# Performance work log

Hardware: AMD Instinct MI355X
Metric: run time of the kernel (lower is better)

The kernel has to match this reference:

```python
import jax, jax.numpy as jnp
import numpy as np

KH, KW = 5, 5  # filter_size


def setup_inputs() -> dict:
    key = jax.random.key(0)
    k1, k2 = jax.random.split(key)
    n, c, t, h, w = 1, 3, 25, 128, 128
    filter_prod = KH * KW  # 25
    up_sq = 16
    x = jax.random.normal(k1, (n, c, t, h, w), dtype=jnp.float32)
    filters = jax.random.uniform(k2, (n, filter_prod, up_sq, t, h, w), dtype=jnp.float32)
    return {"x": x, "filters": filters}


def reference(x, filters):
    # x: (n, 3, t, h, w); filters: (n, kh*kw, up_sq, t, h, w)
    n, c, t, h, w = x.shape
    up_sq = filters.shape[2]
    ph, pw = KH // 2, KW // 2
    # The torch module's 25 one-hot grouped conv2d calls are exactly im2col:
    # patch k = a*KW + b is x shifted by (a-ph, b-pw) with zero padding.
    xp = jnp.pad(x, ((0, 0), (0, 0), (0, 0), (ph, ph), (pw, pw)))
    patches = jnp.stack(
        [xp[:, :, :, a:a + h, b:b + w] for a in range(KH) for b in range(KW)],
        axis=-1,
    )  # (n, 3, t, h, w, kh*kw)
    out = jnp.einsum('ncthwk,nkuthw->ncuthw', patches, filters)
    # (n, 3, up_sq, t, h, w) -> (n, 3*up_sq, t, h, w)
    return out.reshape(n, c * up_sq, t, h, w)
```

## Files before the change

kernel.cpp:

```cpp
#include <hip/hip_runtime.h>


#define T_ 25
#define H_ 128
#define W_ 128
#define C_ 3
#define U_ 16
#define KH_ 5
#define KW_ 5
#define HW_ (H_ * W_)
#define THW_ (T_ * HW_)

#define BLOCK_PIX 256
#define LROWS 6
#define LCOLS 132

__global__ __launch_bounds__(256) void duf_kernel(
    const float* __restrict__ x,
    const float* __restrict__ filt,
    float* __restrict__ out)
{
    __shared__ __align__(16) float xs[C_ * LROWS * LCOLS];

    const int tid = threadIdx.x;
    const int P0  = blockIdx.x * BLOCK_PIX;
    const int t   = P0 / HW_;
    const int h0  = (P0 - t * HW_) / W_;

    const float* xt = x + (size_t)t * HW_;
    for (int idx = tid; idx < C_ * LROWS * LCOLS; idx += 256) {
        const int c   = idx / (LROWS * LCOLS);
        const int rem = idx - c * (LROWS * LCOLS);
        const int r   = rem / LCOLS;
        const int col = rem - r * LCOLS;
        const int gh  = h0 - 2 + r;
        const int gw  = col - 2;
        float v = 0.f;
        if ((unsigned)gh < (unsigned)H_ && (unsigned)gw < (unsigned)W_)
            v = xt[(size_t)c * THW_ + gh * W_ + gw];
        xs[idx] = v;
    }
    __syncthreads();

    const int lane = tid & 63;
    const int uq   = tid >> 6;
    const int p0   = P0 + lane * 4;
    const int lrow = lane >> 5;
    const int w0   = (lane & 31) * 4;

    float4 acc[C_][4];
#pragma unroll
    for (int c = 0; c < C_; ++c)
#pragma unroll
        for (int u = 0; u < 4; ++u)
            acc[c][u] = make_float4(0.f, 0.f, 0.f, 0.f);

    const float* fb = filt + (size_t)(uq * 4) * THW_ + p0;

#pragma unroll 1
    for (int a = 0; a < KH_; ++a) {
        float xr[C_][8];
#pragma unroll
        for (int c = 0; c < C_; ++c) {
            const float4* s =
                (const float4*)&xs[(c * LROWS + lrow + a) * LCOLS + w0];
            const float4 lo = s[0];
            const float4 hi = s[1];
            xr[c][0] = lo.x; xr[c][1] = lo.y; xr[c][2] = lo.z; xr[c][3] = lo.w;
            xr[c][4] = hi.x; xr[c][5] = hi.y; xr[c][6] = hi.z; xr[c][7] = hi.w;
        }
        const float* fa = fb + (size_t)a * (KW_ * U_) * THW_;
#pragma unroll
        for (int b = 0; b < KW_; ++b) {
#pragma unroll
            for (int u = 0; u < 4; ++u) {
                const float4 f =
                    *(const float4*)(fa + (size_t)(b * U_ + u) * THW_);
#pragma unroll
                for (int c = 0; c < C_; ++c) {
                    acc[c][u].x += xr[c][b + 0] * f.x;
                    acc[c][u].y += xr[c][b + 1] * f.y;
                    acc[c][u].z += xr[c][b + 2] * f.z;
                    acc[c][u].w += xr[c][b + 3] * f.w;
                }
            }
        }
    }

#pragma unroll
    for (int c = 0; c < C_; ++c)
#pragma unroll
        for (int u = 0; u < 4; ++u)
            *(float4*)(out + (size_t)(c * U_ + uq * 4 + u) * THW_ + p0) =
                acc[c][u];
}

extern "C" void kernel_launch(void* const* d_in, const int* in_sizes, int n_in,
                              void* d_out, int out_size, void* d_ws, size_t ws_size,
                              hipStream_t stream) {
    const float* x = (const float*)d_in[0];
    const float* filt = (const float*)d_in[1];
    float* out = (float*)d_out;
    dim3 grid(THW_ / BLOCK_PIX);
    dim3 block(256);
    duf_kernel<<<grid, block, 0, stream>>>(x, filt, out);
}
```

Before: 854.4 us.

## Tile 16-row spans per block with one upsample per wave and nontemporal loads

Each block now covers a 16-row span of one frame for a group of four upsample channels, and each wave handles a single upsample channel over eight pixel sub-tiles. Before, each block covered 256 pixels and each wave handled four channels. The x halo in shared memory is reused across more pixels, and the grid shrinks to 800 blocks. Filter loads and output stores now use nontemporal builtins so the large streaming traffic bypasses cache retention. The risks are fewer blocks for the GPU's many CUs, more redundant x halo loads (four channel-group blocks reload the same span), and more registers per thread.

```diff
diff --git a/kernel.cpp b/kernel.cpp
--- a/kernel.cpp
+++ b/kernel.cpp
@@ -1,5 +1,7 @@
 #include <hip/hip_runtime.h>
 
+
+typedef float f4 __attribute__((ext_vector_type(4)));
 
 #define T_ 25
 #define H_ 128
@@ -11,9 +13,11 @@
 #define HW_ (H_ * W_)
 #define THW_ (T_ * HW_)
 
-#define BLOCK_PIX 256
-#define LROWS 6
-#define LCOLS 132
+#define SPAN_ROWS 16
+#define SPAN_PX (SPAN_ROWS * W_)
+#define NSPAN (H_ / SPAN_ROWS)
+#define LROWS (SPAN_ROWS + KH_ - 1)
+#define LCOLS (W_ + 4)
 
 __global__ __launch_bounds__(256) void duf_kernel(
     const float* __restrict__ x,
@@ -22,10 +26,12 @@
 {
     __shared__ __align__(16) float xs[C_ * LROWS * LCOLS];
 
+    const int bid = blockIdx.x;
+    const int ug  = bid & 3;
+    const int sp  = (bid >> 2) & (NSPAN - 1);
+    const int t   = bid >> 5;
+
     const int tid = threadIdx.x;
-    const int P0  = blockIdx.x * BLOCK_PIX;
-    const int t   = P0 / HW_;
-    const int h0  = (P0 - t * HW_) / W_;
 
     const float* xt = x + (size_t)t * HW_;
     for (int idx = tid; idx < C_ * LROWS * LCOLS; idx += 256) {
@@ -33,7 +39,7 @@
         const int rem = idx - c * (LROWS * LCOLS);
         const int r   = rem / LCOLS;
         const int col = rem - r * LCOLS;
-        const int gh  = h0 - 2 + r;
+        const int gh  = sp * SPAN_ROWS - 2 + r;
         const int gw  = col - 2;
         float v = 0.f;
         if ((unsigned)gh < (unsigned)H_ && (unsigned)gw < (unsigned)W_)
@@ -43,56 +49,58 @@
     __syncthreads();
 
     const int lane = tid & 63;
-    const int uq   = tid >> 6;
-    const int p0   = P0 + lane * 4;
+    const int wq   = tid >> 6;
+    const int u    = ug * 4 + wq;
     const int lrow = lane >> 5;
     const int w0   = (lane & 31) * 4;
 
-    float4 acc[C_][4];
+    f4 acc[C_][8];
 #pragma unroll
     for (int c = 0; c < C_; ++c)
 #pragma unroll
-        for (int u = 0; u < 4; ++u)
-            acc[c][u] = make_float4(0.f, 0.f, 0.f, 0.f);
+        for (int j = 0; j < 8; ++j)
+            acc[c][j] = (f4)(0.f);
 
-    const float* fb = filt + (size_t)(uq * 4) * THW_ + p0;
+    const size_t pixbase = (size_t)t * HW_ + (size_t)sp * SPAN_PX + lane * 4;
+    const float* fu = filt + (size_t)u * THW_ + pixbase;
 
 #pragma unroll 1
     for (int a = 0; a < KH_; ++a) {
-        float xr[C_][8];
+        const float* fa = fu + (size_t)(a * KW_) * U_ * THW_;
 #pragma unroll
-        for (int c = 0; c < C_; ++c) {
-            const float4* s =
-                (const float4*)&xs[(c * LROWS + lrow + a) * LCOLS + w0];
-            const float4 lo = s[0];
-            const float4 hi = s[1];
-            xr[c][0] = lo.x; xr[c][1] = lo.y; xr[c][2] = lo.z; xr[c][3] = lo.w;
-            xr[c][4] = hi.x; xr[c][5] = hi.y; xr[c][6] = hi.z; xr[c][7] = hi.w;
-        }
-        const float* fa = fb + (size_t)a * (KW_ * U_) * THW_;
+        for (int j = 0; j < 8; ++j) {
+            float xr[C_][8];
 #pragma unroll
-        for (int b = 0; b < KW_; ++b) {
+            for (int c = 0; c < C_; ++c) {
+                const f4* s = (const f4*)
+                    &xs[(c * LROWS + 2 * j + lrow + a) * LCOLS + w0];
+                const f4 lo = s[0];
+                const f4 hi = s[1];
+                xr[c][0] = lo.x; xr[c][1] = lo.y; xr[c][2] = lo.z; xr[c][3] = lo.w;
+                xr[c][4] = hi.x; xr[c][5] = hi.y; xr[c][6] = hi.z; xr[c][7] = hi.w;
+            }
 #pragma unroll
-            for (int u = 0; u < 4; ++u) {
-                const float4 f =
-                    *(const float4*)(fa + (size_t)(b * U_ + u) * THW_);
+            for (int b = 0; b < KW_; ++b) {
+                const f4 f = __builtin_nontemporal_load(
+                    (const f4*)(fa + (size_t)(b * U_) * THW_ + j * 256));
 #pragma unroll
                 for (int c = 0; c < C_; ++c) {
-                    acc[c][u].x += xr[c][b + 0] * f.x;
-                    acc[c][u].y += xr[c][b + 1] * f.y;
-                    acc[c][u].z += xr[c][b + 2] * f.z;
-                    acc[c][u].w += xr[c][b + 3] * f.w;
+                    acc[c][j].x += xr[c][b + 0] * f.x;
+                    acc[c][j].y += xr[c][b + 1] * f.y;
+                    acc[c][j].z += xr[c][b + 2] * f.z;
+                    acc[c][j].w += xr[c][b + 3] * f.w;
                 }
             }
         }
     }
 
 #pragma unroll
-    for (int c = 0; c < C_; ++c)
+    for (int c = 0; c < C_; ++c) {
+        float* oc = out + (size_t)(c * U_ + u) * THW_ + pixbase;
 #pragma unroll
-        for (int u = 0; u < 4; ++u)
-            *(float4*)(out + (size_t)(c * U_ + uq * 4 + u) * THW_ + p0) =
-                acc[c][u];
+        for (int j = 0; j < 8; ++j)
+            __builtin_nontemporal_store(acc[c][j], (f4*)(oc + j * 256));
+    }
 }
 
 extern "C" void kernel_launch(void* const* d_in, const int* in_sizes, int n_in,
@@ -101,7 +109,7 @@
     const float* x = (const float*)d_in[0];
     const float* filt = (const float*)d_in[1];
     float* out = (float*)d_out;
-    dim3 grid(THW_ / BLOCK_PIX);
+    dim3 grid(T_ * NSPAN * 4);
     dim3 block(256);
     duf_kernel<<<grid, block, 0, stream>>>(x, filt, out);
 }
```

After: 852.2 us. About the same (-0.3%).
